# Performance work log

Measured on AMD Instinct MI355X. Metric: run time of the kernel, lower is better.

The kernel has to match this reference:

```python
import jax, jax.numpy as jnp
import numpy as np

DIM = 256   # model dim (forced by gate Linear(32,4): d = 32 = DIM//H)
H = 8       # heads (hard-coded by mask.repeat(1,8,1,1))
D = DIM // H
B = 256     # batch
NS = 100    # skeleton tokens (sub-block size)
NQ = 64     # query tokens
N = NS + NQ # 164
NE = 4      # experts
HID = 50    # expert hidden
LN_EPS = 1e-5


def setup_inputs() -> dict:
    key = jax.random.key(0)
    ks = jax.random.split(key, 12)
    s = 0.02
    return {
        "x": jax.random.normal(ks[0], (B, N, DIM), jnp.float32),
        "mask": jax.random.randint(ks[1], (B, N), 0, 2).astype(bool),
        "w_qk_s": jax.random.normal(ks[2], (DIM, 2 * DIM), jnp.float32) * s,
        "w_qk_q": jax.random.normal(ks[3], (DIM, 2 * DIM), jnp.float32) * s,
        "w_v": jax.random.normal(ks[4], (DIM, DIM), jnp.float32) * s,
        "w_gate": jax.random.normal(ks[5], (D, NE), jnp.float32) * s,
        "b_gate": jnp.zeros((NE,), jnp.float32),
        "ln_gamma": jnp.ones((NE,), jnp.float32),
        "ln_beta": jnp.zeros((NE,), jnp.float32),
        "w1": jax.random.normal(ks[6], (NE, NS, HID), jnp.float32) * s,
        "b1": jnp.zeros((NE, HID), jnp.float32),
        "w2": jax.random.normal(ks[7], (NE, HID, NS), jnp.float32) * s,
        "b2": jnp.zeros((NE, NS), jnp.float32),
        "w_out": jax.random.normal(ks[8], (DIM, DIM), jnp.float32) * s,
        "b_out": jnp.zeros((DIM,), jnp.float32),
    }


def reference(x, mask, w_qk_s, w_qk_q, w_v, w_gate, b_gate, ln_gamma, ln_beta,
              w1, b1, w2, b2, w_out, b_out):
    b, n, dim = x.shape
    scale = dim ** -0.5  # scale_with_head=False -> dim**-0.5

    def to_heads(t):  # (b, m, H*D) -> (b, H, m, D)
        return t.reshape(b, -1, H, D).transpose(0, 2, 1, 3)

    # separate qk projections for skeleton (first 100) vs query (last 64) tokens
    q_s, k_s = jnp.split(x[:, :NS] @ w_qk_s, 2, axis=-1)
    q_q, k_q = jnp.split(x[:, NS:] @ w_qk_q, 2, axis=-1)
    q = jnp.concatenate([to_heads(q_s), to_heads(q_q)], axis=2)  # (b,H,N,D)
    k = jnp.concatenate([to_heads(k_s), to_heads(k_q)], axis=2)
    v = to_heads(x @ w_v)

    # gates: RAW reshape of x (b,n,H*D) -> (b,H,n,D) (memory reinterpretation,
    # as in torch x.reshape), detached, sliced to first 100 'rows'
    gx = jax.lax.stop_gradient(x).reshape(b, H, n, D)[:, :, :NS, :]
    g = gx @ w_gate + b_gate                              # (b,H,100,4)
    mu = g.mean(-1, keepdims=True)
    var = g.var(-1, keepdims=True)
    g = (g - mu) / jnp.sqrt(var + LN_EPS) * ln_gamma + ln_beta
    gates = jax.nn.softmax(g, axis=-1)                    # (b,H,100,4)

    dots = jnp.einsum('bhid,bhjd->bhij', q, k) * scale    # (b,H,N,N)
    mask_value = -jnp.finfo(dots.dtype).max
    dots = jnp.where(mask[:, None, None, :], mask_value, dots)

    # soft-MoE over the 100x100 sub-block (experts applied along key axis)
    attn_q = dots[:, :, :NS, :NS]                         # (b,H,100,100)
    h1 = jax.nn.relu(jnp.einsum('bhij,ejk->bheik', jax.nn.relu(attn_q), w1)
                     + b1[:, None, :])                    # (b,H,4,100,50)
    eo = jax.nn.relu(jnp.einsum('bheik,ekj->bheij', h1, w2)
                     + b2[:, None, :])                    # (b,H,4,100,100)
    moes = jnp.einsum('bheij,bhie->bhij', eo, gates)      # (b,H,100,100)

    dots = dots.at[:, :, :NS, :NS].add(moes)
    attn = jax.nn.softmax(dots, axis=-1)
    out = jnp.einsum('bhij,bhjd->bhid', attn, v)          # (b,H,N,D)
    out = out.transpose(0, 2, 1, 3).reshape(b, n, dim)
    return out @ w_out + b_out
```

## Files before the change

### kernel.cpp

```cpp
#include <hip/hip_runtime.h>

typedef __bf16 bf16x8 __attribute__((ext_vector_type(8)));
typedef __bf16 bf16x4 __attribute__((ext_vector_type(4)));
typedef float  f32x4  __attribute__((ext_vector_type(4)));

__device__ __forceinline__ bf16x8 ldb8(const __bf16* p) {
    return *reinterpret_cast<const bf16x8*>(p);
}
__device__ __forceinline__ bf16x8 zero8() {
    bf16x8 z;
    #pragma unroll
    for (int i = 0; i < 8; i++) z[i] = (__bf16)0.f;
    return z;
}
__device__ __forceinline__ __bf16 ldw(const void* p, int i, int m) {
    return m ? (__bf16)((const float*)p)[i] : ((const __bf16*)p)[i];
}
__device__ __forceinline__ bf16x8 ldx8(const void* p, size_t ei, int m) {
    if (m) {
        const float* f = (const float*)p + ei;
        f32x4 a = *reinterpret_cast<const f32x4*>(f);
        f32x4 b = *reinterpret_cast<const f32x4*>(f + 4);
        bf16x8 r;
        #pragma unroll
        for (int u = 0; u < 4; u++) { r[u] = (__bf16)a[u]; r[4 + u] = (__bf16)b[u]; }
        return r;
    }
    return ldb8((const __bf16*)p + ei);
}

__global__ __launch_bounds__(256) void prep_kernel(
    const void* x, const void* mask,
    const void* wqks, const void* wqkq, const void* wv, const void* w1,
    const void* w2, const void* wout, const void* wg, const void* bg,
    const void* lng, const void* lnb, const void* b1, const void* b2,
    const void* bout, int* modes, unsigned* maskb,
    __bf16* __restrict__ Wts, __bf16* __restrict__ Wtq,
    __bf16* __restrict__ w1t, __bf16* __restrict__ w2t,
    __bf16* __restrict__ wot, __bf16* __restrict__ wsm)
{
    __shared__ int sbad;
    const int t = threadIdx.x, bid = blockIdx.x;
    if (t == 0) sbad = 0;
    __syncthreads();
    {
        const unsigned int* xw = (const unsigned int*)x;
        int bad = 0;
        for (int i = t; i < 2048; i += 256) {
            unsigned int w = xw[i];
            unsigned int el = (w >> 7) & 0xFF, eh = (w >> 23) & 0xFF;
            if (el >= 0x94 || el == 0xFF) bad++;
            if (eh >= 0x94 || eh == 0xFF) bad++;
        }
        if (bad) atomicAdd(&sbad, bad);
    }
    __syncthreads();
    const int m = (sbad > 64) ? 1 : 0;

    if (bid >= 1268) {
        __shared__ int v32bad, v16bad;
        __shared__ unsigned mb[24];
        const int mbid = bid - 1268;
        if (t == 0) { v32bad = 0; v16bad = 0; }
        if (t < 24) mb[t] = ((t % 6) == 5) ? 0xFFFFFFF0u : 0u;
        __syncthreads();
        const unsigned int* mw = (const unsigned int*)mask;
        int b32 = 0, b16 = 0;
        for (int i = t; i < 10496; i += 256) {
            unsigned int w = mw[i];
            if (!(w == 0u || w == 1u || w == 0x3F800000u)) b32++;
            unsigned int h0 = w & 0xFFFFu, h1 = w >> 16;
            if (!(h0 == 0u || h0 == 1u || h0 == 0x3F80u)) b16++;
            if (!(h1 == 0u || h1 == 1u || h1 == 0x3F80u)) b16++;
        }
        if (b32) atomicAdd(&v32bad, b32);
        if (b16) atomicAdd(&v16bad, b16);
        __syncthreads();
        const int mmode = (v32bad == 0) ? 0 : ((v16bad == 0) ? 2 : 1);
        if (mbid == 0 && t == 0) { modes[0] = m; modes[1] = mmode; }
        const int lo = mbid * 656;
        for (int i2 = t; i2 < 656; i2 += 256) {
            int i = lo + i2;
            int val;
            if (mmode == 0)      val = (((const int*)mask)[i] != 0);
            else if (mmode == 2) val = (((const unsigned short*)mask)[i] != 0);
            else                 val = (((const unsigned char*)mask)[i] != 0);
            if (val) {
                int ib = i2 / 164, jb = i2 - ib * 164;
                atomicOr(&mb[ib * 6 + (jb >> 5)], 1u << (jb & 31));
            }
        }
        __syncthreads();
        if (t < 24) maskb[mbid * 24 + t] = mb[t];
        return;
    }

    int i = bid * 256 + t;
    if (i < 196608) {
        int n = i >> 8, k = i & 255;
        __bf16 vs, vq;
        if (n < 512) { vs = ldw(wqks, k * 512 + n, m); vq = ldw(wqkq, k * 512 + n, m); }
        else         { vs = ldw(wv, k * 256 + (n - 512), m); vq = vs; }
        Wts[i] = vs; Wtq[i] = vq;
        return;
    }
    i -= 196608;
    if (i < 32768) {
        int e = i >> 13, r = i & 8191, n = r >> 7, k = r & 127;
        __bf16 v = (__bf16)0.f;
        if (n < 50) {
            if (k < 100)       v = ldw(w1, (e * 100 + k) * 50 + n, m);
            else if (k == 100) v = ldw(b1, e * 50 + n, m);
        }
        w1t[i] = v;
        return;
    }
    i -= 32768;
    if (i < 28672) {
        int e = i / 7168, r = i % 7168, n = r >> 6, k = r & 63;
        __bf16 v = (__bf16)0.f;
        if (n < 100) {
            if (k < 50)       v = ldw(w2, (e * 50 + k) * 100 + n, m);
            else if (k == 50) v = ldw(b2, e * 100 + n, m);
        }
        w2t[i] = v;
        return;
    }
    i -= 28672;
    if (i < 65536) {
        int n = i >> 8, k = i & 255;
        wot[i] = ldw(wout, k * 256 + n, m);
        return;
    }
    i -= 65536;
    if (i < 996) {
        __bf16 v;
        if (i < 128)      v = ldw(wg, i, m);
        else if (i < 132) v = ldw(bg, i - 128, m);
        else if (i < 136) v = ldw(lng, i - 132, m);
        else if (i < 140) v = ldw(lnb, i - 136, m);
        else if (i < 340) v = ldw(b1, i - 140, m);
        else if (i < 740) v = ldw(b2, i - 340, m);
        else              v = ldw(bout, i - 740, m);
        wsm[i] = v;
    }
}

__global__ __launch_bounds__(256, 2) void qkv_kernel(
    const void* __restrict__ x, const __bf16* __restrict__ Wts,
    const __bf16* __restrict__ Wtq, const __bf16* __restrict__ wsm,
    const int* __restrict__ modes,
    __bf16* __restrict__ q, __bf16* __restrict__ k, __bf16* __restrict__ vt,
    float* __restrict__ gates)
{
    __shared__ __bf16 xs[32][264];
    __shared__ float wgf[128];
    __shared__ float gcst[12];
    const int m = modes[0];
    const int b = blockIdx.y;
    const int mt = blockIdx.x >> 1;
    const int half = blockIdx.x & 1;
    const __bf16* Wt = (mt < 4) ? Wts : Wtq;
    const int rbase = (mt < 4) ? mt * 32 : 100 + (mt - 4) * 32;
    const int tid = threadIdx.x;

    if (tid < 128) wgf[tid] = (float)wsm[tid];
    if (tid < 12)  gcst[tid] = (float)wsm[128 + tid];
    for (int c = tid; c < 1024; c += 256) {
        int row = c >> 5, part = c & 31;
        bf16x8 val = ldx8(x, ((size_t)b * 164 + rbase + row) * 256 + part * 8, m);
        *reinterpret_cast<bf16x8*>(&xs[row][part * 8]) = val;
    }
    __syncthreads();

    if (half == 0) {
        int jg = rbase * 8 + tid;
        int h = jg / 164;
        int j = jg - h * 164;
        if (j < 100) {
            const __bf16* xp = &xs[tid >> 3][(tid & 7) * 32];
            float g[4] = {gcst[0], gcst[1], gcst[2], gcst[3]};
            #pragma unroll
            for (int p = 0; p < 4; p++) {
                bf16x8 xv = ldb8(xp + p * 8);
                #pragma unroll
                for (int u = 0; u < 8; u++) {
                    float f = (float)xv[u];
                    #pragma unroll
                    for (int e = 0; e < 4; e++) g[e] += f * wgf[(p * 8 + u) * 4 + e];
                }
            }
            float mu = 0.25f * (g[0] + g[1] + g[2] + g[3]);
            float var = 0.25f * ((g[0]-mu)*(g[0]-mu) + (g[1]-mu)*(g[1]-mu) +
                                 (g[2]-mu)*(g[2]-mu) + (g[3]-mu)*(g[3]-mu));
            float is = rsqrtf(var + 1e-5f);
            float mx = -3.0e38f;
            #pragma unroll
            for (int e = 0; e < 4; e++) {
                g[e] = (g[e] - mu) * is * gcst[4 + e] + gcst[8 + e];
                mx = fmaxf(mx, g[e]);
            }
            float s = 0.f;
            #pragma unroll
            for (int e = 0; e < 4; e++) { g[e] = __expf(g[e] - mx); s += g[e]; }
            float inv = 1.f / s;
            float4 gv = make_float4(g[0]*inv, g[1]*inv, g[2]*inv, g[3]*inv);
            *reinterpret_cast<float4*>(&gates[((size_t)(b * 8 + h) * 100 + j) * 4]) = gv;
        }
    }

    const int w = tid >> 6, l = tid & 63, lr = l & 15, lc = l >> 4;
    f32x4 acc[2][6];
    #pragma unroll
    for (int ms = 0; ms < 2; ms++)
        #pragma unroll
        for (int nt = 0; nt < 6; nt++) acc[ms][nt] = (f32x4){0.f, 0.f, 0.f, 0.f};

    #pragma unroll
    for (int kt = 0; kt < 8; kt++) {
        bf16x8 a0 = ldb8(&xs[lr][kt * 32 + lc * 8]);
        bf16x8 a1 = ldb8(&xs[16 + lr][kt * 32 + lc * 8]);
        #pragma unroll
        for (int nt = 0; nt < 6; nt++) {
            bf16x8 bb = ldb8(Wt + (size_t)(half * 384 + w * 96 + nt * 16 + lr) * 256 + kt * 32 + lc * 8);
            acc[0][nt] = __builtin_amdgcn_mfma_f32_16x16x32_bf16(a0, bb, acc[0][nt], 0, 0, 0);
            acc[1][nt] = __builtin_amdgcn_mfma_f32_16x16x32_bf16(a1, bb, acc[1][nt], 0, 0, 0);
        }
    }
    #pragma unroll
    for (int ms = 0; ms < 2; ms++) {
        #pragma unroll
        for (int nt = 0; nt < 6; nt++) {
            int c = half * 384 + w * 96 + nt * 16 + lr;
            int i0 = rbase + ms * 16 + lc * 4;
            if (c < 512) {
                __bf16* dst; int ch;
                if (c < 256) { dst = q; ch = c; }
                else         { dst = k; ch = c - 256; }
                int hh = ch >> 5, d = ch & 31;
                #pragma unroll
                for (int r = 0; r < 4; r++) {
                    int i = i0 + r;
                    if (mt >= 4 || i < 100)
                        dst[(((size_t)b * 8 + hh) * 164 + i) * 32 + d] = (__bf16)acc[ms][nt][r];
                }
            } else {
                int ch = c - 512, hh = ch >> 5, d = ch & 31;
                if (mt >= 4 || i0 < 100) {
                    bf16x4 pv;
                    #pragma unroll
                    for (int r = 0; r < 4; r++) pv[r] = (__bf16)acc[ms][nt][r];
                    *reinterpret_cast<bf16x4*>(&vt[((size_t)(b * 8 + hh) * 32 + d) * 176 + i0]) = pv;
                }
            }
        }
    }
}

__global__ __launch_bounds__(256, 4) void attn_kernel(
    const __bf16* __restrict__ qg, const __bf16* __restrict__ kg,
    const __bf16* __restrict__ vtg, const float* __restrict__ gatesg,
    const unsigned* __restrict__ maskbg, const __bf16* __restrict__ w1t,
    const __bf16* __restrict__ w2t, __bf16* __restrict__ ohg)
{
    __shared__ __align__(16) __bf16 lds[19712];
    const int flat = blockIdx.x;
    const int xcd = flat & 7, j5 = flat >> 3;
    const int bh = ((j5 & 255) << 3) | xcd;
    const int rt = j5 >> 8;
    const int b = bh >> 3, tid = threadIdx.x;
    const int w = tid >> 6, l = tid & 63, lr = l & 15, lc = l >> 4;
    const int m0 = w * 16;
    const int WB  = 6400 + w * 3328;
    const int H1B = WB + 2176;
    const bool moe_wave = (rt * 64 + m0) < 100;

    const __bf16* vtb = vtg + (size_t)bh * 32 * 176;
    bf16x8 vv0, vv1, vv2;
    {
        int c = tid;
        int row = c / 24, j0 = (c - row * 24) * 8;
        if (j0 < 164) {
            vv0 = ldb8(vtb + row * 176 + j0);
            if (j0 == 160) { vv0[4] = (__bf16)0.f; vv0[5] = (__bf16)0.f; vv0[6] = (__bf16)0.f; vv0[7] = (__bf16)0.f; }
        } else vv0 = zero8();
    }
    {
        int c = tid + 256;
        int row = c / 24, j0 = (c - row * 24) * 8;
        if (j0 < 164) {
            vv1 = ldb8(vtb + row * 176 + j0);
            if (j0 == 160) { vv1[4] = (__bf16)0.f; vv1[5] = (__bf16)0.f; vv1[6] = (__bf16)0.f; vv1[7] = (__bf16)0.f; }
        } else vv1 = zero8();
    }
    {
        int c = tid + 512;
        int row = c / 24, j0 = (c - row * 24) * 8;
        if (j0 < 164) {
            vv2 = ldb8(vtb + row * 176 + j0);
            if (j0 == 160) { vv2[4] = (__bf16)0.f; vv2[5] = (__bf16)0.f; vv2[6] = (__bf16)0.f; vv2[7] = (__bf16)0.f; }
        } else vv2 = zero8();
    }

    const unsigned* mbp = maskbg + b * 6;
    unsigned mbits = 0;
    #pragma unroll
    for (int nt = 0; nt < 11; nt++)
        mbits |= ((mbp[nt >> 1] >> (((nt & 1) << 4) + lr)) & 1u) << nt;
    int qrow = rt * 64 + m0 + lr; if (qrow > 163) qrow = 163;
    bf16x8 afq = ldb8(qg + ((size_t)bh * 164 + qrow) * 32 + lc * 8);

    const __bf16* kbase = kg + (size_t)bh * 164 * 32;
    f32x4 raw[11];
    #pragma unroll
    for (int nt = 0; nt < 11; nt++) {
        int krow = nt * 16 + lr; if (krow > 163) krow = 163;
        bf16x8 kb = ldb8(kbase + (size_t)krow * 32 + lc * 8);
        f32x4 acc = {0.f, 0.f, 0.f, 0.f};
        acc = __builtin_amdgcn_mfma_f32_16x16x32_bf16(afq, kb, acc, 0, 0, 0);
        bool bad = (mbits >> nt) & 1;
        #pragma unroll
        for (int r = 0; r < 4; r++)
            raw[nt][r] = bad ? -1e30f : acc[r] * 0.0625f;
    }

    {
        int c = tid;
        int row = c / 24, j0 = (c - row * 24) * 8;
        *reinterpret_cast<bf16x8*>(&lds[row * 200 + j0]) = vv0;
        c = tid + 256;
        row = c / 24; j0 = (c - row * 24) * 8;
        *reinterpret_cast<bf16x8*>(&lds[row * 200 + j0]) = vv1;
        c = tid + 512;
        row = c / 24; j0 = (c - row * 24) * 8;
        *reinterpret_cast<bf16x8*>(&lds[row * 200 + j0]) = vv2;
    }

    if (moe_wave) {
        #pragma unroll
        for (int nt = 0; nt < 8; nt++) {
            int j = nt * 16 + lr;
            #pragma unroll
            for (int r = 0; r < 4; r++) {
                float v = raw[nt][r];
                v = (v < 0.f) ? 0.f : v;
                if (j >= 100) v = (j == 100) ? 1.f : 0.f;
                lds[WB + (lc * 4 + r) * 136 + j] = (__bf16)v;
            }
        }
    }

    if (moe_wave) {
        const int gi0 = rt * 64 + m0 + lc * 4;
        for (int e = 0; e < 4; e++) {
            bf16x8 sa[4];
            #pragma unroll
            for (int kt = 0; kt < 4; kt++)
                sa[kt] = ldb8(&lds[WB + lr * 136 + kt * 32 + lc * 8]);
            #pragma unroll
            for (int nt = 0; nt < 4; nt++) {
                f32x4 acc = {0.f, 0.f, 0.f, 0.f};
                __builtin_amdgcn_s_setprio(1);
                #pragma unroll
                for (int kt = 0; kt < 4; kt++) {
                    bf16x8 bb = ldb8(w1t + (size_t)(e * 64 + nt * 16 + lr) * 128 + kt * 32 + lc * 8);
                    acc = __builtin_amdgcn_mfma_f32_16x16x32_bf16(sa[kt], bb, acc, 0, 0, 0);
                }
                __builtin_amdgcn_s_setprio(0);
                int n = nt * 16 + lr;
                #pragma unroll
                for (int r = 0; r < 4; r++) {
                    float v = acc[r];
                    if (v < 0.f) v = 0.f;
                    if (n == 50) v = 1.f;
                    lds[H1B + (lc * 4 + r) * 72 + n] = (__bf16)v;
                }
            }
            bf16x8 ha0 = ldb8(&lds[H1B + lr * 72 + lc * 8]);
            bf16x8 ha1 = ldb8(&lds[H1B + lr * 72 + 32 + lc * 8]);
            float gt[4];
            #pragma unroll
            for (int r = 0; r < 4; r++) {
                int gi = gi0 + r;
                gt[r] = (gi < 100) ? gatesg[((size_t)bh * 100 + gi) * 4 + e] : 0.f;
            }
            #pragma unroll
            for (int nt = 0; nt < 7; nt++) {
                f32x4 acc = {0.f, 0.f, 0.f, 0.f};
                __builtin_amdgcn_s_setprio(1);
                bf16x8 bb0 = ldb8(w2t + (size_t)(e * 112 + nt * 16 + lr) * 64 + lc * 8);
                acc = __builtin_amdgcn_mfma_f32_16x16x32_bf16(ha0, bb0, acc, 0, 0, 0);
                bf16x8 bb1 = ldb8(w2t + (size_t)(e * 112 + nt * 16 + lr) * 64 + 32 + lc * 8);
                acc = __builtin_amdgcn_mfma_f32_16x16x32_bf16(ha1, bb1, acc, 0, 0, 0);
                __builtin_amdgcn_s_setprio(0);
                #pragma unroll
                for (int r = 0; r < 4; r++) {
                    float v = acc[r];
                    if (v < 0.f) v = 0.f;
                    raw[nt][r] += v * gt[r];
                }
            }
        }
    }

    #pragma unroll
    for (int r = 0; r < 4; r++) {
        float m2 = raw[0][r];
        #pragma unroll
        for (int nt = 1; nt < 11; nt++) m2 = fmaxf(m2, raw[nt][r]);
        m2 = fmaxf(m2, __shfl_xor(m2, 1, 64));
        m2 = fmaxf(m2, __shfl_xor(m2, 2, 64));
        m2 = fmaxf(m2, __shfl_xor(m2, 4, 64));
        m2 = fmaxf(m2, __shfl_xor(m2, 8, 64));
        float s2 = 0.f;
        #pragma unroll
        for (int nt = 0; nt < 11; nt++) {
            float ev = __expf(raw[nt][r] - m2);
            raw[nt][r] = ev;
            s2 += ev;
        }
        s2 += __shfl_xor(s2, 1, 64);
        s2 += __shfl_xor(s2, 2, 64);
        s2 += __shfl_xor(s2, 4, 64);
        s2 += __shfl_xor(s2, 8, 64);
        float inv = (s2 > 0.f) ? 1.f / s2 : 0.f;
        #pragma unroll
        for (int nt = 0; nt < 11; nt++)
            lds[WB + (lc * 4 + r) * 200 + nt * 16 + lr] = (__bf16)(raw[nt][r] * inv);
        lds[WB + (lc * 4 + r) * 200 + 176 + lr] = (__bf16)0.f;
    }
    __syncthreads();

    int gi = rt * 64 + m0 + lr;
    #pragma unroll
    for (int nt = 0; nt < 2; nt++) {
        f32x4 acc = {0.f, 0.f, 0.f, 0.f};
        __builtin_amdgcn_s_setprio(1);
        #pragma unroll
        for (int kt = 0; kt < 6; kt++) {
            bf16x8 va = ldb8(&lds[(nt * 16 + lr) * 200 + kt * 32 + lc * 8]);
            bf16x8 pb = ldb8(&lds[WB + lr * 200 + kt * 32 + lc * 8]);
            acc = __builtin_amdgcn_mfma_f32_16x16x32_bf16(va, pb, acc, 0, 0, 0);
        }
        __builtin_amdgcn_s_setprio(0);
        if (gi < 164) {
            bf16x4 ov;
            #pragma unroll
            for (int r = 0; r < 4; r++) ov[r] = (__bf16)acc[r];
            *reinterpret_cast<bf16x4*>(&ohg[((size_t)bh * 164 + gi) * 32 + nt * 16 + lc * 4]) = ov;
        }
    }
}

__global__ __launch_bounds__(256) void outproj_kernel(
    const __bf16* __restrict__ oh, const __bf16* __restrict__ wot,
    const __bf16* __restrict__ wsm, float* __restrict__ out)
{
    const __bf16* bout = wsm + 740;
    const int b = blockIdx.y;
    const int mt = blockIdx.x >> 2;
    const int ntile = blockIdx.x & 3;
    const int tid = threadIdx.x;
    const int w = tid >> 6, l = tid & 63, lr = l & 15, lc = l >> 4;
    int row = mt * 64 + w * 16 + lr; if (row > 163) row = 163;
    f32x4 acc[4];
    #pragma unroll
    for (int nt = 0; nt < 4; nt++) acc[nt] = (f32x4){0.f, 0.f, 0.f, 0.f};
    #pragma unroll
    for (int kt = 0; kt < 8; kt++) {
        bf16x8 a = ldb8(oh + (((size_t)b * 8 + kt) * 164 + row) * 32 + lc * 8);
        #pragma unroll
        for (int nt = 0; nt < 4; nt++) {
            bf16x8 bb = ldb8(wot + (size_t)(ntile * 64 + nt * 16 + lr) * 256 + kt * 32 + lc * 8);
            acc[nt] = __builtin_amdgcn_mfma_f32_16x16x32_bf16(a, bb, acc[nt], 0, 0, 0);
        }
    }
    #pragma unroll
    for (int nt = 0; nt < 4; nt++) {
        int n = ntile * 64 + nt * 16 + lr;
        float bias = (float)bout[n];
        #pragma unroll
        for (int r = 0; r < 4; r++) {
            int i = mt * 64 + w * 16 + lc * 4 + r;
            if (i < 164)
                out[((size_t)b * 164 + i) * 256 + n] = acc[nt][r] + bias;
        }
    }
}

extern "C" void kernel_launch(void* const* d_in, const int* in_sizes, int n_in,
                              void* d_out, int out_size, void* d_ws, size_t ws_size,
                              hipStream_t stream) {
    const void* x      = d_in[0];
    const void* mask   = d_in[1];
    const void* w_qk_s = d_in[2];
    const void* w_qk_q = d_in[3];
    const void* w_v    = d_in[4];
    const void* w_gate = d_in[5];
    const void* b_gate = d_in[6];
    const void* ln_g   = d_in[7];
    const void* ln_b   = d_in[8];
    const void* w1     = d_in[9];
    const void* b1     = d_in[10];
    const void* w2     = d_in[11];
    const void* b2     = d_in[12];
    const void* w_out  = d_in[13];
    const void* b_out  = d_in[14];
    float* out = (float*)d_out;

    char* ws = (char*)d_ws;
    size_t off = 0;
    auto nextp = [&](size_t bytes) {
        char* p = ws + off;
        off += (bytes + 255) & ~(size_t)255;
        return p;
    };
    const size_t QKV_ELEMS = (size_t)256 * 8 * 164 * 32;
    const size_t VT_ELEMS  = (size_t)256 * 8 * 32 * 176;
    int*      modes  = (int*)nextp(64);
    unsigned* maskb  = (unsigned*)nextp((size_t)256 * 6 * 4);
    __bf16* qws  = (__bf16*)nextp(QKV_ELEMS * 2);
    __bf16* kws  = (__bf16*)nextp(QKV_ELEMS * 2);
    __bf16* vtws = (__bf16*)nextp(VT_ELEMS * 2);
    __bf16* ohws = (__bf16*)nextp(QKV_ELEMS * 2);
    float*  gws  = (float*)nextp((size_t)2048 * 100 * 4 * 4);
    __bf16* Wts  = (__bf16*)nextp(768 * 256 * 2);
    __bf16* Wtq  = (__bf16*)nextp(768 * 256 * 2);
    __bf16* w1t  = (__bf16*)nextp(4 * 64 * 128 * 2);
    __bf16* w2t  = (__bf16*)nextp(4 * 112 * 64 * 2);
    __bf16* wot  = (__bf16*)nextp(256 * 256 * 2);
    __bf16* wsm  = (__bf16*)nextp(996 * 2);

    prep_kernel<<<1332, 256, 0, stream>>>(x, mask, w_qk_s, w_qk_q, w_v, w1, w2,
                                          w_out, w_gate, b_gate, ln_g, ln_b, b1,
                                          b2, b_out, modes, maskb,
                                          Wts, Wtq, w1t, w2t, wot, wsm);
    qkv_kernel<<<dim3(12, 256), 256, 0, stream>>>(x, Wts, Wtq, wsm, modes,
                                                  qws, kws, vtws, gws);
    attn_kernel<<<6144, 256, 0, stream>>>(qws, kws, vtws, gws, maskb,
                                          w1t, w2t, ohws);
    outproj_kernel<<<dim3(12, 256), 256, 0, stream>>>(ohws, wot, wsm, out);
}
```

Baseline: 484.5 us.

## Swizzle attention LDS, defer softmax normalization, skip row-max when bounded, rebalance gates

Several unrelated changes land together. The qkv kernel moves the gate computation after the GEMM, splits it across both block halves, and raises the occupancy hint to 3. The attention kernel XOR-swizzles the V and probability LDS layouts to cut bank conflicts, and hoists the MoE A-fragment loads out of the expert loop. The softmax skips the cross-lane row max when every score is at most 8, using a fixed offset of 8 instead, and applies the 1/sum normalization after the PV MFMA. The fixed-offset shortcut assumes bounded scores and could underflow or lose precision for rows whose values are all very negative.

```diff
diff --git a/kernel.cpp b/kernel.cpp
--- a/kernel.cpp
+++ b/kernel.cpp
@@ -146,7 +146,7 @@
     }
 }
 
-__global__ __launch_bounds__(256, 2) void qkv_kernel(
+__global__ __launch_bounds__(256, 3) void qkv_kernel(
     const void* __restrict__ x, const __bf16* __restrict__ Wts,
     const __bf16* __restrict__ Wtq, const __bf16* __restrict__ wsm,
     const int* __restrict__ modes,
@@ -172,42 +172,6 @@
         *reinterpret_cast<bf16x8*>(&xs[row][part * 8]) = val;
     }
     __syncthreads();
-
-    if (half == 0) {
-        int jg = rbase * 8 + tid;
-        int h = jg / 164;
-        int j = jg - h * 164;
-        if (j < 100) {
-            const __bf16* xp = &xs[tid >> 3][(tid & 7) * 32];
-            float g[4] = {gcst[0], gcst[1], gcst[2], gcst[3]};
-            #pragma unroll
-            for (int p = 0; p < 4; p++) {
-                bf16x8 xv = ldb8(xp + p * 8);
-                #pragma unroll
-                for (int u = 0; u < 8; u++) {
-                    float f = (float)xv[u];
-                    #pragma unroll
-                    for (int e = 0; e < 4; e++) g[e] += f * wgf[(p * 8 + u) * 4 + e];
-                }
-            }
-            float mu = 0.25f * (g[0] + g[1] + g[2] + g[3]);
-            float var = 0.25f * ((g[0]-mu)*(g[0]-mu) + (g[1]-mu)*(g[1]-mu) +
-                                 (g[2]-mu)*(g[2]-mu) + (g[3]-mu)*(g[3]-mu));
-            float is = rsqrtf(var + 1e-5f);
-            float mx = -3.0e38f;
-            #pragma unroll
-            for (int e = 0; e < 4; e++) {
-                g[e] = (g[e] - mu) * is * gcst[4 + e] + gcst[8 + e];
-                mx = fmaxf(mx, g[e]);
-            }
-            float s = 0.f;
-            #pragma unroll
-            for (int e = 0; e < 4; e++) { g[e] = __expf(g[e] - mx); s += g[e]; }
-            float inv = 1.f / s;
-            float4 gv = make_float4(g[0]*inv, g[1]*inv, g[2]*inv, g[3]*inv);
-            *reinterpret_cast<float4*>(&gates[((size_t)(b * 8 + h) * 100 + j) * 4]) = gv;
-        }
-    }
 
     const int w = tid >> 6, l = tid & 63, lr = l & 15, lc = l >> 4;
     f32x4 acc[2][6];
@@ -255,6 +219,42 @@
             }
         }
     }
+
+    if ((tid >> 7) == half) {
+        int jg = rbase * 8 + tid;
+        int h = jg / 164;
+        int j = jg - h * 164;
+        if (j < 100) {
+            const __bf16* xp = &xs[tid >> 3][(tid & 7) * 32];
+            float g[4] = {gcst[0], gcst[1], gcst[2], gcst[3]};
+            #pragma unroll
+            for (int p = 0; p < 4; p++) {
+                bf16x8 xv = ldb8(xp + p * 8);
+                #pragma unroll
+                for (int u = 0; u < 8; u++) {
+                    float f = (float)xv[u];
+                    #pragma unroll
+                    for (int e = 0; e < 4; e++) g[e] += f * wgf[(p * 8 + u) * 4 + e];
+                }
+            }
+            float mu = 0.25f * (g[0] + g[1] + g[2] + g[3]);
+            float var = 0.25f * ((g[0]-mu)*(g[0]-mu) + (g[1]-mu)*(g[1]-mu) +
+                                 (g[2]-mu)*(g[2]-mu) + (g[3]-mu)*(g[3]-mu));
+            float is = rsqrtf(var + 1e-5f);
+            float mx = -3.0e38f;
+            #pragma unroll
+            for (int e = 0; e < 4; e++) {
+                g[e] = (g[e] - mu) * is * gcst[4 + e] + gcst[8 + e];
+                mx = fmaxf(mx, g[e]);
+            }
+            float s = 0.f;
+            #pragma unroll
+            for (int e = 0; e < 4; e++) { g[e] = __expf(g[e] - mx); s += g[e]; }
+            float inv = 1.f / s;
+            float4 gv = make_float4(g[0]*inv, g[1]*inv, g[2]*inv, g[3]*inv);
+            *reinterpret_cast<float4*>(&gates[((size_t)(b * 8 + h) * 100 + j) * 4]) = gv;
+        }
+    }
 }
 
 __global__ __launch_bounds__(256, 4) void attn_kernel(
@@ -327,13 +327,13 @@
     {
         int c = tid;
         int row = c / 24, j0 = (c - row * 24) * 8;
-        *reinterpret_cast<bf16x8*>(&lds[row * 200 + j0]) = vv0;
+        *reinterpret_cast<bf16x8*>(&lds[row * 200 + (j0 ^ ((row & 7) << 3))]) = vv0;
         c = tid + 256;
         row = c / 24; j0 = (c - row * 24) * 8;
-        *reinterpret_cast<bf16x8*>(&lds[row * 200 + j0]) = vv1;
+        *reinterpret_cast<bf16x8*>(&lds[row * 200 + (j0 ^ ((row & 7) << 3))]) = vv1;
         c = tid + 512;
         row = c / 24; j0 = (c - row * 24) * 8;
-        *reinterpret_cast<bf16x8*>(&lds[row * 200 + j0]) = vv2;
+        *reinterpret_cast<bf16x8*>(&lds[row * 200 + (j0 ^ ((row & 7) << 3))]) = vv2;
     }
 
     if (moe_wave) {
@@ -352,11 +352,11 @@
 
     if (moe_wave) {
         const int gi0 = rt * 64 + m0 + lc * 4;
+        bf16x8 sa[4];
+        #pragma unroll
+        for (int kt = 0; kt < 4; kt++)
+            sa[kt] = ldb8(&lds[WB + lr * 136 + kt * 32 + lc * 8]);
         for (int e = 0; e < 4; e++) {
-            bf16x8 sa[4];
-            #pragma unroll
-            for (int kt = 0; kt < 4; kt++)
-                sa[kt] = ldb8(&lds[WB + lr * 136 + kt * 32 + lc * 8]);
             #pragma unroll
             for (int nt = 0; nt < 4; nt++) {
                 f32x4 acc = {0.f, 0.f, 0.f, 0.f};
@@ -403,15 +403,25 @@
         }
     }
 
+    float mx = -3.0e38f;
+    #pragma unroll
+    for (int nt = 0; nt < 11; nt++)
+        #pragma unroll
+        for (int r = 0; r < 4; r++) mx = fmaxf(mx, raw[nt][r]);
+    const bool fast = __all(mx <= 8.f) && __any(mx > -1e29f);
+    float s2v0, s2v1, s2v2, s2v3;
     #pragma unroll
     for (int r = 0; r < 4; r++) {
-        float m2 = raw[0][r];
-        #pragma unroll
-        for (int nt = 1; nt < 11; nt++) m2 = fmaxf(m2, raw[nt][r]);
-        m2 = fmaxf(m2, __shfl_xor(m2, 1, 64));
-        m2 = fmaxf(m2, __shfl_xor(m2, 2, 64));
-        m2 = fmaxf(m2, __shfl_xor(m2, 4, 64));
-        m2 = fmaxf(m2, __shfl_xor(m2, 8, 64));
+        float m2 = 8.f;
+        if (!fast) {
+            m2 = raw[0][r];
+            #pragma unroll
+            for (int nt = 1; nt < 11; nt++) m2 = fmaxf(m2, raw[nt][r]);
+            m2 = fmaxf(m2, __shfl_xor(m2, 1, 64));
+            m2 = fmaxf(m2, __shfl_xor(m2, 2, 64));
+            m2 = fmaxf(m2, __shfl_xor(m2, 4, 64));
+            m2 = fmaxf(m2, __shfl_xor(m2, 8, 64));
+        }
         float s2 = 0.f;
         #pragma unroll
         for (int nt = 0; nt < 11; nt++) {
@@ -423,12 +433,19 @@
         s2 += __shfl_xor(s2, 2, 64);
         s2 += __shfl_xor(s2, 4, 64);
         s2 += __shfl_xor(s2, 8, 64);
-        float inv = (s2 > 0.f) ? 1.f / s2 : 0.f;
+        if (r == 0) s2v0 = s2; else if (r == 1) s2v1 = s2;
+        else if (r == 2) s2v2 = s2; else s2v3 = s2;
+        const int rowp = lc * 4 + r;
+        const int key = (rowp & 7) << 3;
         #pragma unroll
         for (int nt = 0; nt < 11; nt++)
-            lds[WB + (lc * 4 + r) * 200 + nt * 16 + lr] = (__bf16)(raw[nt][r] * inv);
-        lds[WB + (lc * 4 + r) * 200 + 176 + lr] = (__bf16)0.f;
-    }
+            lds[WB + rowp * 200 + ((nt * 16 + lr) ^ key)] = (__bf16)raw[nt][r];
+        lds[WB + rowp * 200 + ((176 + lr) ^ key)] = (__bf16)0.f;
+    }
+    float vsel = (lr & 3) == 0 ? s2v0 : (lr & 3) == 1 ? s2v1
+               : (lr & 3) == 2 ? s2v2 : s2v3;
+    float s2row = __shfl(vsel, (lr >> 2) * 16 + lr, 64);
+    float invr = (s2row > 0.f) ? (1.f / s2row) : 0.f;
     __syncthreads();
 
     int gi = rt * 64 + m0 + lr;
@@ -438,15 +455,17 @@
         __builtin_amdgcn_s_setprio(1);
         #pragma unroll
         for (int kt = 0; kt < 6; kt++) {
-            bf16x8 va = ldb8(&lds[(nt * 16 + lr) * 200 + kt * 32 + lc * 8]);
-            bf16x8 pb = ldb8(&lds[WB + lr * 200 + kt * 32 + lc * 8]);
+            int rowv = nt * 16 + lr;
+            int col = kt * 32 + lc * 8;
+            bf16x8 va = ldb8(&lds[rowv * 200 + (col ^ ((rowv & 7) << 3))]);
+            bf16x8 pb = ldb8(&lds[WB + lr * 200 + (col ^ ((lr & 7) << 3))]);
             acc = __builtin_amdgcn_mfma_f32_16x16x32_bf16(va, pb, acc, 0, 0, 0);
         }
         __builtin_amdgcn_s_setprio(0);
         if (gi < 164) {
             bf16x4 ov;
             #pragma unroll
-            for (int r = 0; r < 4; r++) ov[r] = (__bf16)acc[r];
+            for (int r = 0; r < 4; r++) ov[r] = (__bf16)(acc[r] * invr);
             *reinterpret_cast<bf16x4*>(&ohg[((size_t)bh * 164 + gi) * 32 + nt * 16 + lc * 4]) = ov;
         }
     }
```

Result: no change. 486.1 us (+0.3%).
